# Kernel tuning notes

Measured on AMD Instinct MI355X. Metric: run time of the kernel, lower is better.

## Reference

```python
import jax, jax.numpy as jnp
import numpy as np

N_NODES = 50000
N_USERS = 10000
N_STATE = 1024
N_T1 = 2048
N_T2 = 2048
N_EDGES = 4096


def setup_inputs() -> dict:
    key = jax.random.key(0)
    ks = jax.random.split(key, 10)
    d = N_STATE
    s_u = jax.random.normal(ks[0], (N_USERS, d), jnp.float32)
    x = jax.random.normal(ks[1], (N_NODES, d), jnp.float32)
    # Deterministic graph on which the original torch code is well-defined:
    # POI node 0 has one outgoing edge (edge 0) to tail node 1.
    # Tail node 1 receives edges from heads [0, 2, 3, ..., N_EDGES] in edge order,
    # so list-order in the torch loop aligns with edge-index order.
    heads = np.concatenate([[0], np.arange(2, N_EDGES + 1)]).astype(np.int64)
    tails = np.ones(N_EDGES, dtype=np.int64)
    edge_index = jnp.asarray(np.stack([heads, tails]))
    edge_attr = jax.random.normal(ks[2], (N_EDGES, d), jnp.float32)
    T = jax.random.normal(ks[3], (N_T1, N_T2), jnp.float32)
    u = lambda k, s: jax.random.uniform(k, s, jnp.float32, -1.0, 1.0)
    W_u = u(ks[4], (d, 1))
    W_p = u(ks[5], (d, 1))
    W_T_1 = u(ks[6], (d, N_T1))
    W_T_2 = u(ks[7], (N_T2, 1))
    b_T = u(ks[8], (d, 1))
    W_p_ = u(ks[9], (1, d))
    return dict(s_u=s_u, x=x, edge_attr=edge_attr, T=T, W_u=W_u, W_p=W_p,
                W_T_1=W_T_1, W_T_2=W_T_2, b_T=b_T, W_p_=W_p_,
                edge_index=edge_index, user_index=7, POI_index=0)


def reference(s_u, x, edge_attr, T, W_u, W_p, W_T_1, W_T_2, b_T, W_p_,
              edge_index, user_index, POI_index):
    N, d = x.shape
    heads, tails = edge_index[0], edge_index[1]
    # temporal context vector: sigmoid(W_T_1 @ T @ W_T_2 + b_T), shape (d,)
    t_vec = jax.nn.sigmoid(W_T_1 @ T @ W_T_2 + b_T)[:, 0]
    cur_user = s_u[user_index]   # (d,)
    cur_POI = x[POI_index]       # (d,)
    # user update: u' = sigmoid(u + W_u * (h_P . T'))
    s_u = s_u.at[user_index].set(
        jax.nn.sigmoid(cur_user + W_u[:, 0] * jnp.dot(cur_POI, t_vec)))
    # visited POI update: h' = sigmoid(h + W_p * (u . T'))
    new_POI = jax.nn.sigmoid(cur_POI + W_p[:, 0] * jnp.dot(cur_user, t_vec))
    x = x.at[POI_index].set(new_POI)
    # tail entities of the visited POI: x[tail] = new_POI + edge_attr[e]
    rel_mask = heads == POI_index
    dummy = jnp.zeros((1, d), x.dtype)
    tgt = jnp.where(rel_mask, tails, N)  # route masked-out edges to dummy row
    x = jnp.concatenate([x, dummy], 0).at[tgt].set(new_POI[None, :] + edge_attr)[:N]
    # neighboring POIs: edges whose tail is in the tail set; replicate the original
    # neigh_rel[POI_index] = False / neigh_index.remove(POI_index) pair, which by
    # construction both drop the edge at position POI_index.
    is_tail = jnp.zeros((N + 1,), bool).at[tgt].set(True)[:N]
    neigh_mask = is_tail[tails].at[POI_index].set(False)  # (E,)
    h_emb = x[heads]                        # (E, d), tail-updated embeddings
    scal = (h_emb - edge_attr) @ W_p_[0]    # (E,)  W_p_ . (x[head] - r)
    vals = jax.nn.sigmoid(h_emb + scal[:, None])
    tgt2 = jnp.where(neigh_mask, heads, N)
    x = jnp.concatenate([x, dummy], 0).at[tgt2].set(vals)[:N]
    return (s_u, x)
```

## Files before the change

kernel.cpp:

```cpp
#include <hip/hip_runtime.h>
#include <math.h>
#include <limits.h>

#define D 1024

typedef float f32x4 __attribute__((ext_vector_type(4)));

__device__ __forceinline__ float sigmoidf_(float v) {
    return 1.0f / (1.0f + expf(-v));
}

__device__ __forceinline__ float block_reduce_sum256(float v) {
    #pragma unroll
    for (int off = 32; off; off >>= 1) v += __shfl_down(v, off, 64);
    __shared__ float sm[4];
    int lane = threadIdx.x & 63, w = threadIdx.x >> 6;
    if (lane == 0) sm[w] = v;
    __syncthreads();
    float s = sm[0] + sm[1] + sm[2] + sm[3];
    __syncthreads();
    return s;
}

__global__ void k_pre(const float* __restrict__ T,
                      const float* __restrict__ w,
                      float* __restrict__ tmp,
                      const int* __restrict__ edge_index,
                      const int* __restrict__ POI_ptr,
                      int* __restrict__ tail_edge,
                      int* __restrict__ neigh_edge,
                      int n_rows, int E, int t4 ) {
    const int b = blockIdx.x;
    const int tid = threadIdx.x;
    if (b < n_rows) {
        const float4* Tr = (const float4*)(T + (size_t)b * (size_t)(t4 * 4));
        const float4* wv = (const float4*)w;
        float acc = 0.f;
        for (int i = tid; i < t4; i += 256) {
            float4 a = Tr[i], c = wv[i];
            acc += a.x * c.x + a.y * c.y + a.z * c.z + a.w * c.w;
        }
        float s = block_reduce_sum256(acc);
        if (tid == 0) tmp[b] = s;
        return;
    }
    const int POI = POI_ptr[0];
    for (int e = tid; e < E; e += 256)
        if (edge_index[e] == POI) atomicMax(&tail_edge[edge_index[E + e]], e);
    __syncthreads();
    for (int e = tid; e < E; e += 256) {
        if (e == POI) continue;
        int te = atomicMax(&tail_edge[edge_index[E + e]], INT_MIN);
        if (te >= 0) atomicMax(&neigh_edge[edge_index[e]], e);
    }
}

__global__ void k_tvec2(const float* __restrict__ W_T_1,
                        const float* __restrict__ tmp,
                        const float* __restrict__ b_T,
                        const float* __restrict__ x,
                        const float* __restrict__ s_u,
                        const int* __restrict__ user_ptr,
                        const int* __restrict__ POI_ptr,
                        float* __restrict__ pu_P,
                        float* __restrict__ pu_U,
                        int k4 ) {
    const int row = blockIdx.x;
    const float4* Wr = (const float4*)(W_T_1 + (size_t)row * (size_t)(k4 * 4));
    const float4* tv = (const float4*)tmp;
    float acc = 0.f;
    for (int i = threadIdx.x; i < k4; i += 256) {
        float4 a = Wr[i], c = tv[i];
        acc += a.x * c.x + a.y * c.y + a.z * c.z + a.w * c.w;
    }
    float s = block_reduce_sum256(acc);
    if (threadIdx.x == 0) {
        float t = sigmoidf_(s + b_T[row]);
        pu_P[row] = x[(size_t)POI_ptr[0] * D + row] * t;
        pu_U[row] = s_u[(size_t)user_ptr[0] * D + row] * t;
    }
}

__global__ void k_mega(const float* __restrict__ s_u,
                       const float* __restrict__ x,
                       const float* __restrict__ edge_attr,
                       const float* __restrict__ W_u,
                       const float* __restrict__ W_p,
                       const float* __restrict__ Wp_row,
                       const int* __restrict__ user_ptr,
                       const int* __restrict__ POI_ptr,
                       const int* __restrict__ tail_edge,
                       const int* __restrict__ neigh_edge,
                       const float* __restrict__ pu_P,
                       const float* __restrict__ pu_U,
                       float* __restrict__ out,
                       int N_users, int E) {
    const int r = blockIdx.x;
    const int tid = threadIdx.x;

    if (r < N_users) {
        if (r == user_ptr[0]) {
            float4 pp = ((const float4*)pu_P)[tid];
            float dotP = block_reduce_sum256(pp.x + pp.y + pp.z + pp.w);
            float4 uv = ((const float4*)(s_u + (size_t)r * D))[tid];
            float4 wu = ((const float4*)W_u)[tid];
            float4 o;
            o.x = sigmoidf_(uv.x + wu.x * dotP);
            o.y = sigmoidf_(uv.y + wu.y * dotP);
            o.z = sigmoidf_(uv.z + wu.z * dotP);
            o.w = sigmoidf_(uv.w + wu.w * dotP);
            ((float4*)(out + (size_t)r * D))[tid] = o;
        } else {
            const f32x4* src = (const f32x4*)(s_u + (size_t)r * D);
            f32x4* dst = (f32x4*)(out + (size_t)r * D);
            f32x4 v = __builtin_nontemporal_load(&src[tid]);
            __builtin_nontemporal_store(v, &dst[tid]);
        }
        return;
    }

    const int j = r - N_users;
    const int ne = neigh_edge[j];
    const int te = tail_edge[j];
    const int POI = POI_ptr[0];

    if (ne < 0 && te < 0 && j != POI) {
        const f32x4* src = (const f32x4*)(x + (size_t)j * D);
        f32x4* dst = (f32x4*)(out + (size_t)r * D);
        f32x4 v = __builtin_nontemporal_load(&src[tid]);
        __builtin_nontemporal_store(v, &dst[tid]);
        return;
    }

    float4 uu = ((const float4*)pu_U)[tid];
    float dotU = block_reduce_sum256(uu.x + uu.y + uu.z + uu.w);
    float4 xp = ((const float4*)(x + (size_t)POI * D))[tid];
    float4 wp = ((const float4*)W_p)[tid];
    float4 np;
    np.x = sigmoidf_(xp.x + wp.x * dotU);
    np.y = sigmoidf_(xp.y + wp.y * dotU);
    np.z = sigmoidf_(xp.z + wp.z * dotU);
    np.w = sigmoidf_(xp.w + wp.w * dotU);

    float4 hv;
    if (te >= 0) {
        float4 b = ((const float4*)(edge_attr + (size_t)te * D))[tid];
        hv = make_float4(np.x + b.x, np.y + b.y, np.z + b.z, np.w + b.w);
    } else if (j == POI) {
        hv = np;
    } else {
        hv = ((const float4*)(x + (size_t)j * D))[tid];
    }

    float4* dst = (float4*)(out + (size_t)r * D);
    if (ne < 0) {
        dst[tid] = hv;
        return;
    }

    float4 ev = ((const float4*)(edge_attr + (size_t)ne * D))[tid];
    float4 w = ((const float4*)Wp_row)[tid];
    float acc = (hv.x - ev.x) * w.x + (hv.y - ev.y) * w.y +
                (hv.z - ev.z) * w.z + (hv.w - ev.w) * w.w;
    float scal = block_reduce_sum256(acc);
    float4 o;
    o.x = sigmoidf_(hv.x + scal);
    o.y = sigmoidf_(hv.y + scal);
    o.z = sigmoidf_(hv.z + scal);
    o.w = sigmoidf_(hv.w + scal);
    dst[tid] = o;
}

extern "C" void kernel_launch(void* const* d_in, const int* in_sizes, int n_in,
                              void* d_out, int out_size, void* d_ws, size_t ws_size,
                              hipStream_t stream) {
    const float* s_u       = (const float*)d_in[0];
    const float* x         = (const float*)d_in[1];
    const float* edge_attr = (const float*)d_in[2];
    const float* T         = (const float*)d_in[3];
    const float* W_u       = (const float*)d_in[4];
    const float* W_p       = (const float*)d_in[5];
    const float* W_T_1     = (const float*)d_in[6];
    const float* W_T_2     = (const float*)d_in[7];
    const float* b_T       = (const float*)d_in[8];
    const float* W_p_      = (const float*)d_in[9];
    const int*   edge_index = (const int*)d_in[10];
    const int*   user_ptr   = (const int*)d_in[11];
    const int*   POI_ptr    = (const int*)d_in[12];

    const int E       = in_sizes[10] / 2;
    const int N_users = in_sizes[0] / D;
    const int N       = in_sizes[1] / D;
    const int N_T2    = in_sizes[7];
    const int N_T1    = in_sizes[6] / D;

    float* ws_f       = (float*)d_ws;
    float* tmp        = ws_f;
    float* pu_P       = ws_f + N_T1;
    float* pu_U       = pu_P + D;
    int*   tail_edge  = (int*)(pu_U + D);
    int*   neigh_edge = tail_edge + N;

    hipMemsetAsync(tail_edge, 0xFF, sizeof(int) * (size_t)(2 * N), stream);

    k_pre<<<N_T1 + 1, 256, 0, stream>>>(T, W_T_2, tmp, edge_index, POI_ptr,
                                        tail_edge, neigh_edge, N_T1, E, N_T2 / 4);
    k_tvec2<<<D, 256, 0, stream>>>(W_T_1, tmp, b_T, x, s_u, user_ptr, POI_ptr,
                                   pu_P, pu_U, N_T1 / 4);
    k_mega<<<N_users + N, 256, 0, stream>>>(s_u, x, edge_attr, W_u, W_p, W_p_,
                                            user_ptr, POI_ptr, tail_edge,
                                            neigh_edge, pu_P, pu_U,
                                            (float*)d_out, N_users, E);
}
```

Before: 113.1 us.

## Fold flag init into GEMV kernel, move graph scan, batch 8 rows per block

```diff
diff --git a/kernel.cpp b/kernel.cpp
--- a/kernel.cpp
+++ b/kernel.cpp
@@ -25,34 +25,23 @@
 __global__ void k_pre(const float* __restrict__ T,
                       const float* __restrict__ w,
                       float* __restrict__ tmp,
-                      const int* __restrict__ edge_index,
-                      const int* __restrict__ POI_ptr,
-                      int* __restrict__ tail_edge,
-                      int* __restrict__ neigh_edge,
-                      int n_rows, int E, int t4 ) {
-    const int b = blockIdx.x;
+                      int* __restrict__ flags,
+                      int n_flags, int t4 ) {
     const int tid = threadIdx.x;
-    if (b < n_rows) {
-        const float4* Tr = (const float4*)(T + (size_t)b * (size_t)(t4 * 4));
-        const float4* wv = (const float4*)w;
-        float acc = 0.f;
-        for (int i = tid; i < t4; i += 256) {
-            float4 a = Tr[i], c = wv[i];
-            acc += a.x * c.x + a.y * c.y + a.z * c.z + a.w * c.w;
-        }
-        float s = block_reduce_sum256(acc);
-        if (tid == 0) tmp[b] = s;
-        return;
-    }
-    const int POI = POI_ptr[0];
-    for (int e = tid; e < E; e += 256)
-        if (edge_index[e] == POI) atomicMax(&tail_edge[edge_index[E + e]], e);
-    __syncthreads();
-    for (int e = tid; e < E; e += 256) {
-        if (e == POI) continue;
-        int te = atomicMax(&tail_edge[edge_index[E + e]], INT_MIN);
-        if (te >= 0) atomicMax(&neigh_edge[edge_index[e]], e);
-    }
+    int gid = blockIdx.x * 256 + tid;
+    int gsz = gridDim.x * 256;
+    for (int i = gid; i < n_flags; i += gsz) flags[i] = -1;
+
+    const int row = blockIdx.x;
+    const float4* Tr = (const float4*)(T + (size_t)row * (size_t)(t4 * 4));
+    const float4* wv = (const float4*)w;
+    float acc = 0.f;
+    for (int i = tid; i < t4; i += 256) {
+        float4 a = Tr[i], c = wv[i];
+        acc += a.x * c.x + a.y * c.y + a.z * c.z + a.w * c.w;
+    }
+    float s = block_reduce_sum256(acc);
+    if (tid == 0) tmp[row] = s;
 }
 
 __global__ void k_tvec2(const float* __restrict__ W_T_1,
@@ -62,113 +51,143 @@
                         const float* __restrict__ s_u,
                         const int* __restrict__ user_ptr,
                         const int* __restrict__ POI_ptr,
+                        const int* __restrict__ edge_index,
+                        int* __restrict__ tail_edge,
+                        int* __restrict__ neigh_edge,
                         float* __restrict__ pu_P,
                         float* __restrict__ pu_U,
-                        int k4 ) {
+                        int k4 , int E) {
+    const int tid = threadIdx.x;
+    if (blockIdx.x == gridDim.x - 1) {
+        const int POI = POI_ptr[0];
+        for (int e = tid; e < E; e += 256)
+            if (edge_index[e] == POI)
+                atomicMax(&tail_edge[edge_index[E + e]], e);
+        __syncthreads();
+        for (int e = tid; e < E; e += 256) {
+            if (e == POI) continue;
+            int te = atomicMax(&tail_edge[edge_index[E + e]], INT_MIN);
+            if (te >= 0) atomicMax(&neigh_edge[edge_index[e]], e);
+        }
+        return;
+    }
     const int row = blockIdx.x;
     const float4* Wr = (const float4*)(W_T_1 + (size_t)row * (size_t)(k4 * 4));
     const float4* tv = (const float4*)tmp;
     float acc = 0.f;
-    for (int i = threadIdx.x; i < k4; i += 256) {
+    for (int i = tid; i < k4; i += 256) {
         float4 a = Wr[i], c = tv[i];
         acc += a.x * c.x + a.y * c.y + a.z * c.z + a.w * c.w;
     }
     float s = block_reduce_sum256(acc);
-    if (threadIdx.x == 0) {
+    if (tid == 0) {
         float t = sigmoidf_(s + b_T[row]);
         pu_P[row] = x[(size_t)POI_ptr[0] * D + row] * t;
         pu_U[row] = s_u[(size_t)user_ptr[0] * D + row] * t;
     }
 }
 
-__global__ void k_mega(const float* __restrict__ s_u,
-                       const float* __restrict__ x,
-                       const float* __restrict__ edge_attr,
-                       const float* __restrict__ W_u,
-                       const float* __restrict__ W_p,
-                       const float* __restrict__ Wp_row,
-                       const int* __restrict__ user_ptr,
-                       const int* __restrict__ POI_ptr,
-                       const int* __restrict__ tail_edge,
-                       const int* __restrict__ neigh_edge,
-                       const float* __restrict__ pu_P,
-                       const float* __restrict__ pu_U,
-                       float* __restrict__ out,
-                       int N_users, int E) {
-    const int r = blockIdx.x;
+__global__ void k_mega8(const float* __restrict__ s_u,
+                        const float* __restrict__ x,
+                        const float* __restrict__ edge_attr,
+                        const float* __restrict__ W_u,
+                        const float* __restrict__ W_p,
+                        const float* __restrict__ Wp_row,
+                        const int* __restrict__ user_ptr,
+                        const int* __restrict__ POI_ptr,
+                        const int* __restrict__ tail_edge,
+                        const int* __restrict__ neigh_edge,
+                        const float* __restrict__ pu_P,
+                        const float* __restrict__ pu_U,
+                        float* __restrict__ out,
+                        int N_users, int total_rows) {
     const int tid = threadIdx.x;
-
-    if (r < N_users) {
-        if (r == user_ptr[0]) {
-            float4 pp = ((const float4*)pu_P)[tid];
+    const int base = blockIdx.x * 8;
+    const int user = user_ptr[0], POI = POI_ptr[0];
+
+    f32x4 v[8];
+    #pragma unroll
+    for (int k = 0; k < 8; k++) {
+        int r = base + k;
+        if (r >= total_rows) continue;
+        const float* src = (r < N_users) ? s_u + (size_t)r * D
+                                         : x + (size_t)(r - N_users) * D;
+        v[k] = __builtin_nontemporal_load((const f32x4*)src + tid);
+    }
+
+    int te[8], ne[8];
+    bool sp[8];
+    #pragma unroll
+    for (int k = 0; k < 8; k++) {
+        int r = base + k;
+        te[k] = -1; ne[k] = -1; sp[k] = false;
+        if (r >= total_rows) continue;
+        if (r < N_users) {
+            sp[k] = (r == user);
+        } else {
+            int j = r - N_users;
+            te[k] = tail_edge[j];
+            ne[k] = neigh_edge[j];
+            sp[k] = (te[k] >= 0) || (ne[k] >= 0) || (j == POI);
+        }
+    }
+
+    #pragma unroll
+    for (int k = 0; k < 8; k++) {
+        int r = base + k;
+        if (r >= total_rows) continue;
+        f32x4* dst = (f32x4*)(out + (size_t)r * D) + tid;
+        if (!sp[k]) {
+            __builtin_nontemporal_store(v[k], dst);
+            continue;
+        }
+        if (r < N_users) {
+            f32x4 pp = ((const f32x4*)pu_P)[tid];
             float dotP = block_reduce_sum256(pp.x + pp.y + pp.z + pp.w);
-            float4 uv = ((const float4*)(s_u + (size_t)r * D))[tid];
-            float4 wu = ((const float4*)W_u)[tid];
-            float4 o;
-            o.x = sigmoidf_(uv.x + wu.x * dotP);
-            o.y = sigmoidf_(uv.y + wu.y * dotP);
-            o.z = sigmoidf_(uv.z + wu.z * dotP);
-            o.w = sigmoidf_(uv.w + wu.w * dotP);
-            ((float4*)(out + (size_t)r * D))[tid] = o;
+            f32x4 wu = ((const f32x4*)W_u)[tid];
+            f32x4 o;
+            o.x = sigmoidf_(v[k].x + wu.x * dotP);
+            o.y = sigmoidf_(v[k].y + wu.y * dotP);
+            o.z = sigmoidf_(v[k].z + wu.z * dotP);
+            o.w = sigmoidf_(v[k].w + wu.w * dotP);
+            __builtin_nontemporal_store(o, dst);
+            continue;
+        }
+        const int j = r - N_users;
+        f32x4 uu = ((const f32x4*)pu_U)[tid];
+        float dotU = block_reduce_sum256(uu.x + uu.y + uu.z + uu.w);
+        f32x4 xp = ((const f32x4*)(x + (size_t)POI * D))[tid];
+        f32x4 wp = ((const f32x4*)W_p)[tid];
+        f32x4 np;
+        np.x = sigmoidf_(xp.x + wp.x * dotU);
+        np.y = sigmoidf_(xp.y + wp.y * dotU);
+        np.z = sigmoidf_(xp.z + wp.z * dotU);
+        np.w = sigmoidf_(xp.w + wp.w * dotU);
+        f32x4 hv;
+        if (te[k] >= 0) {
+            f32x4 b = ((const f32x4*)(edge_attr + (size_t)te[k] * D))[tid];
+            hv = np + b;
+        } else if (j == POI) {
+            hv = np;
         } else {
-            const f32x4* src = (const f32x4*)(s_u + (size_t)r * D);
-            f32x4* dst = (f32x4*)(out + (size_t)r * D);
-            f32x4 v = __builtin_nontemporal_load(&src[tid]);
-            __builtin_nontemporal_store(v, &dst[tid]);
-        }
-        return;
-    }
-
-    const int j = r - N_users;
-    const int ne = neigh_edge[j];
-    const int te = tail_edge[j];
-    const int POI = POI_ptr[0];
-
-    if (ne < 0 && te < 0 && j != POI) {
-        const f32x4* src = (const f32x4*)(x + (size_t)j * D);
-        f32x4* dst = (f32x4*)(out + (size_t)r * D);
-        f32x4 v = __builtin_nontemporal_load(&src[tid]);
-        __builtin_nontemporal_store(v, &dst[tid]);
-        return;
-    }
-
-    float4 uu = ((const float4*)pu_U)[tid];
-    float dotU = block_reduce_sum256(uu.x + uu.y + uu.z + uu.w);
-    float4 xp = ((const float4*)(x + (size_t)POI * D))[tid];
-    float4 wp = ((const float4*)W_p)[tid];
-    float4 np;
-    np.x = sigmoidf_(xp.x + wp.x * dotU);
-    np.y = sigmoidf_(xp.y + wp.y * dotU);
-    np.z = sigmoidf_(xp.z + wp.z * dotU);
-    np.w = sigmoidf_(xp.w + wp.w * dotU);
-
-    float4 hv;
-    if (te >= 0) {
-        float4 b = ((const float4*)(edge_attr + (size_t)te * D))[tid];
-        hv = make_float4(np.x + b.x, np.y + b.y, np.z + b.z, np.w + b.w);
-    } else if (j == POI) {
-        hv = np;
-    } else {
-        hv = ((const float4*)(x + (size_t)j * D))[tid];
-    }
-
-    float4* dst = (float4*)(out + (size_t)r * D);
-    if (ne < 0) {
-        dst[tid] = hv;
-        return;
-    }
-
-    float4 ev = ((const float4*)(edge_attr + (size_t)ne * D))[tid];
-    float4 w = ((const float4*)Wp_row)[tid];
-    float acc = (hv.x - ev.x) * w.x + (hv.y - ev.y) * w.y +
-                (hv.z - ev.z) * w.z + (hv.w - ev.w) * w.w;
-    float scal = block_reduce_sum256(acc);
-    float4 o;
-    o.x = sigmoidf_(hv.x + scal);
-    o.y = sigmoidf_(hv.y + scal);
-    o.z = sigmoidf_(hv.z + scal);
-    o.w = sigmoidf_(hv.w + scal);
-    dst[tid] = o;
+            hv = v[k];
+        }
+        if (ne[k] < 0) {
+            __builtin_nontemporal_store(hv, dst);
+            continue;
+        }
+        f32x4 ev = ((const f32x4*)(edge_attr + (size_t)ne[k] * D))[tid];
+        f32x4 w = ((const f32x4*)Wp_row)[tid];
+        f32x4 dd = hv - ev;
+        float acc = dd.x * w.x + dd.y * w.y + dd.z * w.z + dd.w * w.w;
+        float scal = block_reduce_sum256(acc);
+        f32x4 o;
+        o.x = sigmoidf_(hv.x + scal);
+        o.y = sigmoidf_(hv.y + scal);
+        o.z = sigmoidf_(hv.z + scal);
+        o.w = sigmoidf_(hv.w + scal);
+        __builtin_nontemporal_store(o, dst);
+    }
 }
 
 extern "C" void kernel_launch(void* const* d_in, const int* in_sizes, int n_in,
@@ -201,14 +220,14 @@
     int*   tail_edge  = (int*)(pu_U + D);
     int*   neigh_edge = tail_edge + N;
 
-    hipMemsetAsync(tail_edge, 0xFF, sizeof(int) * (size_t)(2 * N), stream);
-
-    k_pre<<<N_T1 + 1, 256, 0, stream>>>(T, W_T_2, tmp, edge_index, POI_ptr,
-                                        tail_edge, neigh_edge, N_T1, E, N_T2 / 4);
-    k_tvec2<<<D, 256, 0, stream>>>(W_T_1, tmp, b_T, x, s_u, user_ptr, POI_ptr,
-                                   pu_P, pu_U, N_T1 / 4);
-    k_mega<<<N_users + N, 256, 0, stream>>>(s_u, x, edge_attr, W_u, W_p, W_p_,
-                                            user_ptr, POI_ptr, tail_edge,
-                                            neigh_edge, pu_P, pu_U,
-                                            (float*)d_out, N_users, E);
-}
+    k_pre<<<N_T1, 256, 0, stream>>>(T, W_T_2, tmp, tail_edge, 2 * N, N_T2 / 4);
+
+    k_tvec2<<<D + 1, 256, 0, stream>>>(W_T_1, tmp, b_T, x, s_u, user_ptr,
+                                       POI_ptr, edge_index, tail_edge,
+                                       neigh_edge, pu_P, pu_U, N_T1 / 4, E);
+
+    const int total_rows = N_users + N;
+    k_mega8<<<(total_rows + 7) / 8, 256, 0, stream>>>(
+        s_u, x, edge_attr, W_u, W_p, W_p_, user_ptr, POI_ptr,
+        tail_edge, neigh_edge, pu_P, pu_U, (float*)d_out, N_users, total_rows);
+}
```

Result: faster. 109.2 us (median of 2 runs) (-3.5%).
